# Kernel tuning notes

Hardware: AMD Instinct MI355X
Metric: run time of the kernel (lower is better)

The kernel has to match this reference:

```python
import jax, jax.numpy as jnp
import numpy as np
import math

# Config constants (match init_kwargs)
E = 8          # n_experts
TOPK = 2       # attn_topk
DIM = 1024     # transformer_dim
B = 4          # batch_size
S = 1024       # max_seq_len
H = 1024       # num_heads * head_dim
SCALE = 1.0 / math.sqrt(DIM)  # original divides scores by sqrt(self.dim)


def setup_inputs() -> dict:
    key = jax.random.key(0)
    ks = jax.random.split(key, 8)
    w = 0.02  # weight init scale
    return {
        "X": jax.random.normal(ks[0], (B, S, DIM), jnp.float32),
        "mask": jnp.ones((B, S), jnp.float32),
        "switch_W": jax.random.normal(ks[1], (DIM * S, E), jnp.float32) * w,
        "switch_b": jnp.zeros((E,), jnp.float32),
        "Wq": jax.random.normal(ks[2], (E, DIM, H), jnp.float32) * w,
        "bq": jnp.zeros((E, H), jnp.float32),
        "Wk": jax.random.normal(ks[3], (E, DIM, H), jnp.float32) * w,
        "bk": jnp.zeros((E, H), jnp.float32),
        "Wv": jax.random.normal(ks[4], (E, DIM, H), jnp.float32) * w,
        "bv": jnp.zeros((E, H), jnp.float32),
        "Wff": jax.random.normal(ks[5], (E, H, DIM), jnp.float32) * w,
        "bff": jnp.zeros((E, DIM), jnp.float32),
    }


def _dispatch_mask(route_prob):
    # top-k expert routing per batch element -> hard {0,1} mask [B, E]
    _, idx = jax.lax.top_k(route_prob, TOPK)  # [B, TOPK]
    b = route_prob.shape[0]
    return jnp.zeros((b, E), route_prob.dtype).at[jnp.arange(b)[:, None], idx].set(1.0)


def reference(X, mask, switch_W, switch_b, Wq, bq, Wk, bk, Wv, bv, Wff, bff):
    b, s, d = X.shape
    # Router: Linear(dim*seq_len -> n_experts) + softmax; preprocess -> idx_list
    logits = X.reshape(b, -1) @ switch_W + switch_b          # [B, E]
    route_prob = jax.nn.softmax(logits, axis=-1)
    m = _dispatch_mask(route_prob)                            # [B, E] dispatch mask (idx_list)

    # Per-expert Q/K/V projections (ColumnParallelLinearWithMoE over routed batches)
    Q = jnp.einsum('bsd,edh->ebsh', X, Wq) + bq[:, None, None, :]  # [E,B,S,H]
    K = jnp.einsum('bsd,edh->ebsh', X, Wk) + bk[:, None, None, :]
    V = jnp.einsum('bsd,edh->ebsh', X, Wv) + bv[:, None, None, :]

    # RowParallelMatmulWithMoE: per-expert scores, softmax (dropout p=0)
    scores = jnp.einsum('ebsh,ebth->ebst', Q, K) * SCALE      # [E,B,S,S]
    P = jax.nn.softmax(scores, axis=-1)

    # index_add_ combine of per-expert attn maps (second preprocess reuses same routing)
    A = jnp.einsum('be,ebst->bst', m, P)                      # [B,S,S]

    # ColumnParallelMatmulWithMoE: attn @ V per expert
    ctx = jnp.einsum('bst,ebth->ebsh', A, V)                  # [E,B,S,H]

    # RowParallelLinearWithMoE output projection, then index_add_ combine
    out = jnp.einsum('ebsh,ehd->ebsd', ctx, Wff) + bff[:, None, None, :]
    y = jnp.einsum('be,ebsd->bsd', m, out)                    # [B,S,DIM]
    return y
```

## Files before the change

### kernel.cpp

```cpp
#include <hip/hip_runtime.h>
#include <math.h>

typedef unsigned short u16;
typedef __attribute__((ext_vector_type(8))) short bffrag;
typedef __attribute__((ext_vector_type(4))) float f32x4;
typedef __attribute__((ext_vector_type(4))) unsigned short us4;
typedef __attribute__((ext_vector_type(8))) unsigned short us8;

#define SCALE_QK (1.0f/32.0f)

__device__ __forceinline__ u16 f2bf(float f) {
    unsigned u = __builtin_bit_cast(unsigned, f);
    u += 0x7fffu + ((u >> 16) & 1u);
    return (u16)(u >> 16);
}
__device__ __forceinline__ float bf2f(u16 v) {
    unsigned u = ((unsigned)v) << 16;
    return __builtin_bit_cast(float, u);
}

__device__ __forceinline__ void gld16(const u16* g, u16* l) {
    __builtin_amdgcn_global_load_lds(
        (const __attribute__((address_space(1))) void*)g,
        (__attribute__((address_space(3))) void*)l, 16, 0, 0);
}

__global__ __launch_bounds__(256) void router_partial(const float* __restrict__ X,
                                                      const float* __restrict__ sW,
                                                      float* __restrict__ part) {
    float acc[32];
    #pragma unroll
    for (int a = 0; a < 32; ++a) acc[a] = 0.f;
    int tid = blockIdx.x * 256 + threadIdx.x;
    #pragma unroll
    for (int q = 0; q < 4; ++q) {
        int i = tid + q * 262144;
        float4 w0 = *(const float4*)(sW + (size_t)i * 8);
        float4 w1 = *(const float4*)(sW + (size_t)i * 8 + 4);
        #pragma unroll
        for (int b = 0; b < 4; ++b) {
            float x = X[((size_t)b << 20) + i];
            acc[b*8+0] += x * w0.x; acc[b*8+1] += x * w0.y;
            acc[b*8+2] += x * w0.z; acc[b*8+3] += x * w0.w;
            acc[b*8+4] += x * w1.x; acc[b*8+5] += x * w1.y;
            acc[b*8+6] += x * w1.z; acc[b*8+7] += x * w1.w;
        }
    }
    __shared__ float wsum[4][32];
    int lane = threadIdx.x & 63, wv = threadIdx.x >> 6;
    #pragma unroll
    for (int a = 0; a < 32; ++a) {
        float v = acc[a];
        #pragma unroll
        for (int off = 32; off; off >>= 1) v += __shfl_down(v, off, 64);
        if (lane == 0) wsum[wv][a] = v;
    }
    __syncthreads();
    int t = threadIdx.x;
    if (t < 32)
        part[(size_t)t * 1024 + blockIdx.x] = wsum[0][t] + wsum[1][t] + wsum[2][t] + wsum[3][t];
}

__global__ __launch_bounds__(256) void router_final(const float* __restrict__ part,
                                                    const float* __restrict__ sb,
                                                    int* __restrict__ sel_need) {
    __shared__ float ps[32][8];
    __shared__ float lg[32];
    int t = threadIdx.x, a = t >> 3, c = t & 7;
    {
        float s = 0.f;
        const float* p = part + (size_t)a * 1024 + c * 128;
        for (int i = 0; i < 128; ++i) s += p[i];
        ps[a][c] = s;
    }
    __syncthreads();
    if (t < 32) {
        float v = 0.f;
        #pragma unroll
        for (int j = 0; j < 8; ++j) v += ps[t][j];
        lg[t] = v + sb[t & 7];
    }
    __syncthreads();
    if (t < 4) {
        int base = t * 8;
        int e1 = 0; float v1 = lg[base];
        for (int e = 1; e < 8; ++e) { if (lg[base + e] > v1) { v1 = lg[base + e]; e1 = e; } }
        int e2 = -1; float v2 = -INFINITY;
        for (int e = 0; e < 8; ++e) {
            if (e == e1) continue;
            if (lg[base + e] > v2) { v2 = lg[base + e]; e2 = e; }
        }
        sel_need[t * 2] = e1; sel_need[t * 2 + 1] = e2;
    }
    __syncthreads();
    if (t < 8) {
        int need = 0;
        for (int j = 0; j < 8; ++j) need |= (sel_need[j] == t);
        sel_need[8 + t] = need;
    }
}

__global__ __launch_bounds__(256) void c1_partial(const float* __restrict__ Wff,
        const float* __restrict__ bv, const int* __restrict__ sel_need,
        float* __restrict__ cpart) {
    int e = blockIdx.z;
    if (!sel_need[8 + e]) return;
    int d = blockIdx.x * 256 + threadIdx.x;
    int h0 = blockIdx.y * 128;
    const float* W = Wff + ((size_t)e << 20) + (size_t)h0 * 1024 + d;
    const float* bvp = bv + e * 1024 + h0;
    float s = 0.f;
    #pragma unroll 4
    for (int h = 0; h < 128; ++h) s += bvp[h] * W[(size_t)h * 1024];
    cpart[(e * 8 + blockIdx.y) * 1024 + d] = s;
}

__global__ __launch_bounds__(256) void ybias_kernel(const float* __restrict__ cpart,
        const float* __restrict__ bff, const int* __restrict__ sel,
        float* __restrict__ ybias) {
    int b = blockIdx.y;
    int d = blockIdx.x * 256 + threadIdx.x;
    int e0 = sel[b * 2], e1 = sel[b * 2 + 1];
    float c0 = 0.f, c1v = 0.f;
    #pragma unroll
    for (int hc = 0; hc < 8; ++hc) {
        c0  += cpart[(e0 * 8 + hc) * 1024 + d];
        c1v += cpart[(e1 * 8 + hc) * 1024 + d];
    }
    ybias[b * 1024 + d] = 2.f * (c0 + c1v) + bff[e0 * 1024 + d] + bff[e1 * 1024 + d];
}

__global__ __launch_bounds__(256) void cvt_misc(const float* __restrict__ X,
                                                const float* __restrict__ Wv,
                                                const int* __restrict__ sel_need,
                                                u16* __restrict__ Xb, u16* __restrict__ WvB) {
    int yz = blockIdx.y;
    const float* src; u16* dst;
    if (yz < 4) {
        src = X + ((size_t)yz << 20);  dst = Xb + ((size_t)yz << 20);
    } else {
        int e = yz - 4;
        if (!sel_need[8 + e]) return;
        src = Wv + ((size_t)e << 20);  dst = WvB + ((size_t)e << 20);
    }
    size_t i = (size_t)(blockIdx.x * 256 + threadIdx.x) * 8;
    float4 a = *(const float4*)(src + i);
    float4 b = *(const float4*)(src + i + 4);
    us8 o;
    o[0] = f2bf(a.x); o[1] = f2bf(a.y); o[2] = f2bf(a.z); o[3] = f2bf(a.w);
    o[4] = f2bf(b.x); o[5] = f2bf(b.y); o[6] = f2bf(b.z); o[7] = f2bf(b.w);
    *(us8*)(dst + i) = o;
}

__global__ __launch_bounds__(256) void cvt_wt(const float* __restrict__ Wq,
                                              const float* __restrict__ Wk,
                                              const float* __restrict__ Wff,
                                              const int* __restrict__ sel_need,
                                              u16* __restrict__ WqT, u16* __restrict__ WkT,
                                              u16* __restrict__ WffT) {
    int z = blockIdx.z;
    int type = z >> 3, e = z & 7;
    if (!sel_need[8 + e]) return;
    const float* src = (type == 0 ? Wq : type == 1 ? Wk : Wff) + ((size_t)e << 20);
    u16* dst = (type == 0 ? WqT : type == 1 ? WkT : WffT) + ((size_t)e << 20);
    __shared__ u16 lt[128 * 136];
    int R0 = blockIdx.y * 128, C0 = blockIdx.x * 128;
    int t = threadIdx.x;
    int c = t & 127;
    int rh = (t >> 7) * 4;
    #pragma unroll
    for (int it = 0; it < 16; ++it) {
        int r4 = it * 8 + rh;
        us4 o;
        #pragma unroll
        for (int j = 0; j < 4; ++j)
            o[j] = f2bf(src[(size_t)(R0 + r4 + j) * 1024 + C0 + c]);
        *(us4*)&lt[c * 136 + r4] = o;
    }
    __syncthreads();
    int dd = (t & 15) * 8;
    int hh = t >> 4;
    #pragma unroll
    for (int it = 0; it < 8; ++it) {
        int cr = it * 16 + hh;
        us8 o = *(const us8*)&lt[cr * 136 + dd];
        *(us8*)(dst + (size_t)(C0 + cr) * 1024 + R0 + dd) = o;
    }
}

__device__ __forceinline__ void stage_half8(const u16* g, int ld, u16* ldst, int tid) {
    int r = tid >> 3;
    int j = ((tid ^ r) & 7) * 8;
    gld16(g + (size_t)r * ld + j, ldst + tid * 8);
    gld16(g + (size_t)(r + 64) * ld + j, ldst + 4096 + tid * 8);
}

template<int Q, bool LASTVM>
__device__ __forceinline__ void phase8(const u16* Ac, const bffrag (&bfr)[4][2],
                                       f32x4 (&acc)[8][4], int rb, int l15, int x0,
                                       const u16* sg, int sld, u16* sdst, int tid) {
    bffrag af[2][2];
    #pragma unroll
    for (int mm = 0; mm < 2; ++mm) {
        int r = (rb + Q * 32 + mm * 16 + l15) * 64;
        af[mm][0] = *(const bffrag*)(Ac + r + x0);
        af[mm][1] = *(const bffrag*)(Ac + r + (x0 ^ 32));
    }
    __builtin_amdgcn_sched_barrier(0);
    stage_half8(sg, sld, sdst, tid);
    __builtin_amdgcn_sched_barrier(0);
    __builtin_amdgcn_s_barrier();
    asm volatile("s_waitcnt lgkmcnt(0)" ::: "memory");
    __builtin_amdgcn_sched_barrier(0);
    __builtin_amdgcn_s_setprio(1);
    #pragma unroll
    for (int ks = 0; ks < 2; ++ks)
        #pragma unroll
        for (int mm = 0; mm < 2; ++mm)
            #pragma unroll
            for (int nn = 0; nn < 4; ++nn)
                acc[Q*2+mm][nn] = __builtin_amdgcn_mfma_f32_16x16x32_bf16(
                    af[mm][ks], bfr[nn][ks], acc[Q*2+mm][nn], 0, 0, 0);
    __builtin_amdgcn_s_setprio(0);
    __builtin_amdgcn_sched_barrier(0);
    if (LASTVM) asm volatile("s_waitcnt vmcnt(4)" ::: "memory");
    __builtin_amdgcn_s_barrier();
}

__device__ __forceinline__ void gemm8(const u16* __restrict__ A, int lda,
                                      const u16* __restrict__ B, int ldb,
                                      int K, f32x4 (&acc)[8][4]) {
    __shared__ u16 lds[65536];
    const int tid = threadIdx.x, l = tid & 63, wid = tid >> 6;
    const int wr = wid >> 2, wc = wid & 3;
    const int l15 = l & 15;
    const int rb = wr * 128;
    const int cb = wc * 64;
    const int x0 = (((l >> 4) ^ (l & 7)) * 8);
    const int m0 = blockIdx.y * 256, n0 = blockIdx.x * 256;
    const int nt = K >> 6;

    const u16* Ag = A + (size_t)m0 * lda;
    const u16* Bg = B + (size_t)n0 * ldb;

    stage_half8(Ag,                          lda, lds,                 tid);
    stage_half8(Ag + (size_t)128 * lda,      lda, lds + 8192,          tid);
    stage_half8(Bg,                          ldb, lds + 16384,         tid);
    stage_half8(Bg + (size_t)128 * ldb,      ldb, lds + 16384 + 8192,  tid);
    stage_half8(Bg + 64,                     ldb, lds + 32768 + 16384, tid);
    stage_half8(Bg + 64 + (size_t)128 * ldb, ldb, lds + 32768 + 16384 + 8192, tid);
    asm volatile("s_waitcnt vmcnt(4)" ::: "memory");
    __builtin_amdgcn_s_barrier();

    for (int t7 = 0; t7 < nt; ++t7) {
        const int cur = t7 & 1;
        u16* Ac = lds + cur * 32768;
        u16* Bc = Ac + 16384;
        u16* An = lds + (cur ^ 1) * 32768;
        const int ka = (t7 + 1 < nt ? t7 + 1 : nt - 1) << 6;
        const int kb = (t7 + 2 < nt ? t7 + 2 : nt - 1) << 6;
        const u16* sA0 = Ag + ka;
        const u16* sA1 = Ag + (size_t)128 * lda + ka;
        const u16* sB0 = Bg + kb;
        const u16* sB1 = Bg + (size_t)128 * ldb + kb;

        bffrag bfr[4][2];
        #pragma unroll
        for (int nn = 0; nn < 4; ++nn) {
            int r = (cb + nn * 16 + l15) * 64;
            bfr[nn][0] = *(const bffrag*)(Bc + r + x0);
            bfr[nn][1] = *(const bffrag*)(Bc + r + (x0 ^ 32));
        }
        phase8<0, false>(Ac, bfr, acc, rb, l15, x0, sA0, lda, An, tid);
        phase8<1, false>(Ac, bfr, acc, rb, l15, x0, sA1, lda, An + 8192, tid);
        phase8<2, false>(Ac, bfr, acc, rb, l15, x0, sB0, ldb, Bc, tid);
        phase8<3, true >(Ac, bfr, acc, rb, l15, x0, sB1, ldb, Bc + 8192, tid);
    }
}

__device__ __forceinline__ void zero8(f32x4 (&acc)[8][4]) {
    #pragma unroll
    for (int m = 0; m < 8; ++m)
        #pragma unroll
        for (int n = 0; n < 4; ++n)
            #pragma unroll
            for (int i = 0; i < 4; ++i) acc[m][n][i] = 0.f;
}

__device__ __forceinline__ void epi8_bf16(u16* __restrict__ C, int ldc, float scale,
                                          const f32x4 (&acc)[8][4],
                                          const float* __restrict__ biasN) {
    const int tid = threadIdx.x, l = tid & 63, wid = tid >> 6;
    const int wr = wid >> 2, wc = wid & 3;
    const int m0 = blockIdx.y * 256 + wr * 128, n0 = blockIdx.x * 256 + wc * 64;
    const int l15 = l & 15, l4 = (l >> 4) * 4;
    #pragma unroll
    for (int mt = 0; mt < 8; ++mt)
        #pragma unroll
        for (int nn = 0; nn < 4; ++nn) {
            int col = n0 + nn * 16 + l15;
            float bn = biasN ? biasN[col] : 0.f;
            #pragma unroll
            for (int i = 0; i < 4; ++i) {
                int row = m0 + mt * 16 + l4 + i;
                C[(size_t)row * ldc + col] = f2bf(acc[mt][nn][i] * scale + bn);
            }
        }
}

__global__ __launch_bounds__(512) void mfma8_qk(const u16* __restrict__ Xb,
        const u16* __restrict__ WqT, const u16* __restrict__ WkT,
        const float* __restrict__ bq, const float* __restrict__ bk,
        const int* __restrict__ sel, u16* __restrict__ Qb, u16* __restrict__ Kb) {
    int z = blockIdx.z, w = z >> 3, bs = z & 7;
    int b = bs >> 1, e = sel[bs];
    f32x4 acc[8][4]; zero8(acc);
    gemm8(Xb + ((size_t)b << 20), 1024, (w ? WkT : WqT) + ((size_t)e << 20), 1024, 1024, acc);
    epi8_bf16((w ? Kb : Qb) + ((size_t)bs << 20), 1024, 1.0f, acc, (w ? bk : bq) + e * 1024);
}

__global__ __launch_bounds__(512) void mfma8_sw(const u16* __restrict__ Qb,
        const u16* __restrict__ Kb, const u16* __restrict__ WffT,
        const u16* __restrict__ WvB, const int* __restrict__ sel,
        u16* __restrict__ Sb, u16* __restrict__ P0b, u16* __restrict__ P1b) {
    int z = blockIdx.z;
    f32x4 acc[8][4]; zero8(acc);
    if (z < 8) {
        gemm8(Qb + ((size_t)z << 20), 1024, Kb + ((size_t)z << 20), 1024, 1024, acc);
        epi8_bf16(Sb + ((size_t)z << 20), 1024, SCALE_QK, acc, nullptr);
    } else {
        int h = (z >= 12), b = z & 3, e = sel[b * 2 + h];
        gemm8(WffT + ((size_t)e << 20), 1024, WvB + ((size_t)e << 20), 1024, 1024, acc);
        epi8_bf16((h ? P1b : P0b) + ((size_t)b << 20), 1024, 1.0f, acc, nullptr);
    }
}

__global__ __launch_bounds__(256) void wvfadd(const u16* __restrict__ P0b,
                                              const u16* __restrict__ P1b,
                                              u16* __restrict__ W) {
    size_t i = (size_t)(blockIdx.x * 256 + threadIdx.x) * 8;
    us8 a = *(const us8*)(P0b + i);
    us8 b = *(const us8*)(P1b + i);
    us8 o;
    #pragma unroll
    for (int j = 0; j < 8; ++j) o[j] = f2bf(bf2f(a[j]) + bf2f(b[j]));
    *(us8*)(W + i) = o;
}

__device__ __forceinline__ void stage_tile(const u16* a0, const u16* a1,
                                           const u16* b0, const u16* b1,
                                           u16* sa, u16* sb, int tid) {
    gld16(a0, &sa[tid * 8]);
    gld16(a1, &sa[2048 + tid * 8]);
    gld16(b0, &sb[tid * 8]);
    gld16(b1, &sb[2048 + tid * 8]);
}

__device__ __forceinline__ void gemm_ds(const u16* __restrict__ A, int lda,
                                        const u16* __restrict__ B, int ldb,
                                        int K, f32x4 (&acc)[4][4]) {
    __shared__ u16 sA[2][4096];
    __shared__ u16 sB[2][4096];
    const int tid = threadIdx.x, lane = tid & 63, wv = tid >> 6;
    const int wr = (wv >> 1) * 64, wc = (wv & 1) * 64;
    const int l15 = lane & 15, lk = (lane >> 4) * 8;
    const int m0 = blockIdx.y * 128, n0 = blockIdx.x * 128;
    const int r0 = tid >> 2, k8 = (tid & 3) * 8;

    const u16* a0 = A + (size_t)(m0 + r0) * lda + k8;
    const u16* a1 = A + (size_t)(m0 + 64 + r0) * lda + k8;
    const u16* b0 = B + (size_t)(n0 + r0) * ldb + k8;
    const u16* b1 = B + (size_t)(n0 + 64 + r0) * ldb + k8;

    stage_tile(a0, a1, b0, b1, sA[0], sB[0], tid);
    __syncthreads();

    const int nt = K >> 5;
    for (int t = 0; t < nt; ++t) {
        const int cur = t & 1;
        if (t + 1 < nt) {
            int k0 = (t + 1) << 5;
            stage_tile(a0 + k0, a1 + k0, b0 + k0, b1 + k0, sA[cur ^ 1], sB[cur ^ 1], tid);
        }
        bffrag av[4], bf[4];
        #pragma unroll
        for (int m = 0; m < 4; ++m)
            av[m] = *reinterpret_cast<const bffrag*>(&sA[cur][(wr + m * 16 + l15) * 32 + lk]);
        #pragma unroll
        for (int n = 0; n < 4; ++n)
            bf[n] = *reinterpret_cast<const bffrag*>(&sB[cur][(wc + n * 16 + l15) * 32 + lk]);
        #pragma unroll
        for (int m = 0; m < 4; ++m)
            #pragma unroll
            for (int n = 0; n < 4; ++n)
                acc[m][n] = __builtin_amdgcn_mfma_f32_16x16x32_bf16(av[m], bf[n], acc[m][n], 0, 0, 0);
        __syncthreads();
    }
}

__device__ __forceinline__ void zero_acc(f32x4 (&acc)[4][4]) {
    #pragma unroll
    for (int m = 0; m < 4; ++m)
        #pragma unroll
        for (int n = 0; n < 4; ++n)
            #pragma unroll
            for (int i = 0; i < 4; ++i) acc[m][n][i] = 0.f;
}

__device__ __forceinline__ void epilogue_bf16(u16* __restrict__ C, int ldc,
                                              const f32x4 (&acc)[4][4]) {
    const int tid = threadIdx.x, lane = tid & 63, wv = tid >> 6;
    const int wr = (wv >> 1) * 64, wc = (wv & 1) * 64;
    const int m0 = blockIdx.y * 128, n0 = blockIdx.x * 128;
    const int l15 = lane & 15, l4 = (lane >> 4) * 4;
    #pragma unroll
    for (int m = 0; m < 4; ++m)
        #pragma unroll
        for (int n = 0; n < 4; ++n) {
            int col = n0 + wc + n * 16 + l15;
            #pragma unroll
            for (int i = 0; i < 4; ++i) {
                int row = m0 + wr + m * 16 + l4 + i;
                C[(size_t)row * ldc + col] = f2bf(acc[m][n][i]);
            }
        }
}

__device__ __forceinline__ void epilogue_f32(float* __restrict__ C, int ldc,
                                             const f32x4 (&acc)[4][4],
                                             const float* __restrict__ bias1) {
    const int tid = threadIdx.x, lane = tid & 63, wv = tid >> 6;
    const int wr = (wv >> 1) * 64, wc = (wv & 1) * 64;
    const int m0 = blockIdx.y * 128, n0 = blockIdx.x * 128;
    const int l15 = lane & 15, l4 = (lane >> 4) * 4;
    #pragma unroll
    for (int m = 0; m < 4; ++m)
        #pragma unroll
        for (int n = 0; n < 4; ++n) {
            int col = n0 + wc + n * 16 + l15;
            float bn = bias1 ? bias1[col] : 0.f;
            #pragma unroll
            for (int i = 0; i < 4; ++i) {
                int row = m0 + wr + m * 16 + l4 + i;
                C[(size_t)row * ldc + col] = acc[m][n][i] + bn;
            }
        }
}

__global__ __launch_bounds__(256) void sm_combine(const u16* __restrict__ Sb, u16* __restrict__ Ab) {
    int bs = blockIdx.x, b = bs >> 10, s = bs & 1023;
    const u16* S0 = Sb + ((size_t)(b * 2) << 20) + (size_t)s * 1024;
    const u16* S1 = S0 + (1u << 20);
    int t = threadIdx.x, lane = t & 63, wv = t >> 6;
    us4 xv0 = *(const us4*)(S0 + t * 4);
    us4 xv1 = *(const us4*)(S1 + t * 4);
    float x0[4], x1[4];
    #pragma unroll
    for (int j = 0; j < 4; ++j) { x0[j] = bf2f(xv0[j]); x1[j] = bf2f(xv1[j]); }
    float m0 = fmaxf(fmaxf(x0[0], x0[1]), fmaxf(x0[2], x0[3]));
    float m1 = fmaxf(fmaxf(x1[0], x1[1]), fmaxf(x1[2], x1[3]));
    #pragma unroll
    for (int off = 32; off; off >>= 1) {
        m0 = fmaxf(m0, __shfl_xor(m0, off, 64));
        m1 = fmaxf(m1, __shfl_xor(m1, off, 64));
    }
    __shared__ float wred[4][4];
    if (lane == 0) { wred[wv][0] = m0; wred[wv][1] = m1; }
    __syncthreads();
    m0 = fmaxf(fmaxf(wred[0][0], wred[1][0]), fmaxf(wred[2][0], wred[3][0]));
    m1 = fmaxf(fmaxf(wred[0][1], wred[1][1]), fmaxf(wred[2][1], wred[3][1]));
    float e0[4], e1[4];
    #pragma unroll
    for (int j = 0; j < 4; ++j) { e0[j] = __expf(x0[j] - m0); e1[j] = __expf(x1[j] - m1); }
    float s0 = e0[0] + e0[1] + e0[2] + e0[3];
    float s1 = e1[0] + e1[1] + e1[2] + e1[3];
    #pragma unroll
    for (int off = 32; off; off >>= 1) {
        s0 += __shfl_xor(s0, off, 64);
        s1 += __shfl_xor(s1, off, 64);
    }
    if (lane == 0) { wred[wv][2] = s0; wred[wv][3] = s1; }
    __syncthreads();
    s0 = wred[0][2] + wred[1][2] + wred[2][2] + wred[3][2];
    s1 = wred[0][3] + wred[1][3] + wred[2][3] + wred[3][3];
    float r0 = 1.f / s0, r1 = 1.f / s1;
    us4 o;
    #pragma unroll
    for (int j = 0; j < 4; ++j) o[j] = f2bf(e0[j] * r0 + e1[j] * r1);
    *(us4*)(Ab + ((size_t)b << 20) + (size_t)s * 1024 + t * 4) = o;
}

__global__ __launch_bounds__(256) void mfma_mt(const u16* __restrict__ Wvfsum,
        const u16* __restrict__ Xb, u16* __restrict__ Mtb) {
    int b = blockIdx.z;
    f32x4 acc[4][4]; zero_acc(acc);
    gemm_ds(Wvfsum + ((size_t)b << 20), 1024, Xb + ((size_t)b << 20), 1024, 1024, acc);
    epilogue_bf16(Mtb + ((size_t)b << 20), 1024, acc);
}

__global__ __launch_bounds__(256) void mfma_y(const u16* __restrict__ Abf,
        const u16* __restrict__ Mtb, const float* __restrict__ ybias,
        float* __restrict__ y) {
    int b = blockIdx.z;
    f32x4 acc[4][4]; zero_acc(acc);
    gemm_ds(Abf + ((size_t)b << 20), 1024, Mtb + ((size_t)b << 20), 1024, 1024, acc);
    epilogue_f32(y + ((size_t)b << 20), 1024, acc, ybias + b * 1024);
}

extern "C" void kernel_launch(void* const* d_in, const int* in_sizes, int n_in,
                              void* d_out, int out_size, void* d_ws, size_t ws_size,
                              hipStream_t stream) {
    const float* X   = (const float*)d_in[0];
    const float* sW  = (const float*)d_in[2];
    const float* sb  = (const float*)d_in[3];
    const float* Wq  = (const float*)d_in[4];
    const float* bq  = (const float*)d_in[5];
    const float* Wk  = (const float*)d_in[6];
    const float* bk  = (const float*)d_in[7];
    const float* Wv  = (const float*)d_in[8];
    const float* bv  = (const float*)d_in[9];
    const float* Wff = (const float*)d_in[10];
    const float* bff = (const float*)d_in[11];
    float* y = (float*)d_out;

    char* w = (char*)d_ws;
    float* part  = (float*)w;
    float* cpart = (float*)w;
    int*   sel   = (int*)(w + (1u << 18));
    float* ybias = (float*)(w + (1u << 18) + 256);
    u16* base = (u16*)(w + (1u << 19));
    u16* Xb   = base;
    u16* WqT  = Xb   + (4u << 20);
    u16* WkT  = WqT  + (8u << 20);
    u16* WffT = WkT  + (8u << 20);
    u16* WvB  = WffT + (8u << 20);
    u16* Qb   = WvB  + (8u << 20);
    u16* Kb   = Qb   + (8u << 20);
    u16* Sb   = Kb   + (8u << 20);
    u16* P0b  = Sb   + (8u << 20);
    u16* P1b  = P0b  + (4u << 20);
    u16* Abf    = WqT;
    u16* Mtb    = WkT;
    u16* Wvfsum = Qb;

    router_partial<<<1024, 256, 0, stream>>>(X, sW, part);
    router_final<<<1, 256, 0, stream>>>(part, sb, sel);
    c1_partial<<<dim3(4, 8, 8), 256, 0, stream>>>(Wff, bv, sel, cpart);
    ybias_kernel<<<dim3(4, 4), 256, 0, stream>>>(cpart, bff, sel, ybias);
    cvt_misc<<<dim3(512, 12), 256, 0, stream>>>(X, Wv, sel, Xb, WvB);
    cvt_wt<<<dim3(8, 8, 24), 256, 0, stream>>>(Wq, Wk, Wff, sel, WqT, WkT, WffT);

    mfma8_qk<<<dim3(4, 4, 16), 512, 0, stream>>>(Xb, WqT, WkT, bq, bk, sel, Qb, Kb);
    mfma8_sw<<<dim3(4, 4, 16), 512, 0, stream>>>(Qb, Kb, WffT, WvB, sel, Sb, P0b, P1b);
    wvfadd<<<2048, 256, 0, stream>>>(P0b, P1b, Wvfsum);
    mfma_mt<<<dim3(8, 8, 4), 256, 0, stream>>>(Wvfsum, Xb, Mtb);
    sm_combine<<<4096, 256, 0, stream>>>(Sb, Abf);
    mfma_y<<<dim3(8, 8, 4), 256, 0, stream>>>(Abf, Mtb, ybias, y);
}
```

Measured before the change: 221.8 us.

## Fuse two-expert WvWff GEMMs by K-concatenation and halve the gemm8 pipeline phases

The two per-batch expert products WffT·WvB are now computed as one GEMM with K=2048. The K loop switches from the first expert's operands to the second's at a split point, so the summed result is written directly. This removes the separate wvfadd kernel and the P0/P1 intermediate buffers, and shrinks the mfma8_sw grid from 16 to 12 z-slices. The gemm8 main loop also goes from four quarter-tile phases to two full-tile phases, each staging a whole 256-row tile, which means fewer barriers per K step. In exchange, the fused blocks do twice the K work, which lengthens the critical path of that launch, and each phase holds more A fragments in registers.

```diff
diff --git a/kernel.cpp b/kernel.cpp
--- a/kernel.cpp
+++ b/kernel.cpp
@@ -188,26 +188,29 @@
     }
 }
 
-__device__ __forceinline__ void stage_half8(const u16* g, int ld, u16* ldst, int tid) {
+__device__ __forceinline__ void stage_full(const u16* g, int ld, u16* ldst, int tid) {
     int r = tid >> 3;
     int j = ((tid ^ r) & 7) * 8;
-    gld16(g + (size_t)r * ld + j, ldst + tid * 8);
-    gld16(g + (size_t)(r + 64) * ld + j, ldst + 4096 + tid * 8);
-}
-
-template<int Q, bool LASTVM>
-__device__ __forceinline__ void phase8(const u16* Ac, const bffrag (&bfr)[4][2],
+    const u16* gr = g + (size_t)r * ld + j;
+    gld16(gr,                      ldst + tid * 8);
+    gld16(gr + (size_t)64  * ld,   ldst + 4096  + tid * 8);
+    gld16(gr + (size_t)128 * ld,   ldst + 8192  + tid * 8);
+    gld16(gr + (size_t)192 * ld,   ldst + 12288 + tid * 8);
+}
+
+template<int QB, bool LASTVM>
+__device__ __forceinline__ void phaseF(const u16* Ac, const bffrag (&bfr)[4][2],
                                        f32x4 (&acc)[8][4], int rb, int l15, int x0,
                                        const u16* sg, int sld, u16* sdst, int tid) {
-    bffrag af[2][2];
-    #pragma unroll
-    for (int mm = 0; mm < 2; ++mm) {
-        int r = (rb + Q * 32 + mm * 16 + l15) * 64;
+    bffrag af[4][2];
+    #pragma unroll
+    for (int mm = 0; mm < 4; ++mm) {
+        int r = (rb + QB * 64 + mm * 16 + l15) * 64;
         af[mm][0] = *(const bffrag*)(Ac + r + x0);
         af[mm][1] = *(const bffrag*)(Ac + r + (x0 ^ 32));
     }
     __builtin_amdgcn_sched_barrier(0);
-    stage_half8(sg, sld, sdst, tid);
+    stage_full(sg, sld, sdst, tid);
     __builtin_amdgcn_sched_barrier(0);
     __builtin_amdgcn_s_barrier();
     asm volatile("s_waitcnt lgkmcnt(0)" ::: "memory");
@@ -216,19 +219,21 @@
     #pragma unroll
     for (int ks = 0; ks < 2; ++ks)
         #pragma unroll
-        for (int mm = 0; mm < 2; ++mm)
+        for (int mm = 0; mm < 4; ++mm)
             #pragma unroll
             for (int nn = 0; nn < 4; ++nn)
-                acc[Q*2+mm][nn] = __builtin_amdgcn_mfma_f32_16x16x32_bf16(
-                    af[mm][ks], bfr[nn][ks], acc[Q*2+mm][nn], 0, 0, 0);
+                acc[QB*4+mm][nn] = __builtin_amdgcn_mfma_f32_16x16x32_bf16(
+                    af[mm][ks], bfr[nn][ks], acc[QB*4+mm][nn], 0, 0, 0);
     __builtin_amdgcn_s_setprio(0);
     __builtin_amdgcn_sched_barrier(0);
     if (LASTVM) asm volatile("s_waitcnt vmcnt(4)" ::: "memory");
     __builtin_amdgcn_s_barrier();
 }
 
-__device__ __forceinline__ void gemm8(const u16* __restrict__ A, int lda,
-                                      const u16* __restrict__ B, int ldb,
+__device__ __forceinline__ void gemm8(const u16* __restrict__ A0, const u16* __restrict__ A1,
+                                      int asplit, int lda,
+                                      const u16* __restrict__ B0, const u16* __restrict__ B1,
+                                      int bsplit, int ldb,
                                       int K, f32x4 (&acc)[8][4]) {
     __shared__ u16 lds[65536];
     const int tid = threadIdx.x, l = tid & 63, wid = tid >> 6;
@@ -240,15 +245,18 @@
     const int m0 = blockIdx.y * 256, n0 = blockIdx.x * 256;
     const int nt = K >> 6;
 
-    const u16* Ag = A + (size_t)m0 * lda;
-    const u16* Bg = B + (size_t)n0 * ldb;
-
-    stage_half8(Ag,                          lda, lds,                 tid);
-    stage_half8(Ag + (size_t)128 * lda,      lda, lds + 8192,          tid);
-    stage_half8(Bg,                          ldb, lds + 16384,         tid);
-    stage_half8(Bg + (size_t)128 * ldb,      ldb, lds + 16384 + 8192,  tid);
-    stage_half8(Bg + 64,                     ldb, lds + 32768 + 16384, tid);
-    stage_half8(Bg + 64 + (size_t)128 * ldb, ldb, lds + 32768 + 16384 + 8192, tid);
+    const u16* A0g = A0 + (size_t)m0 * lda;
+    const u16* A1g = A1 + (size_t)m0 * lda;
+    const u16* B0g = B0 + (size_t)n0 * ldb;
+    const u16* B1g = B1 + (size_t)n0 * ldb;
+
+    stage_full(A0g, lda, lds,         tid);
+    stage_full(B0g, ldb, lds + 16384, tid);
+    {
+        int kb = (1 < nt ? 1 : nt - 1) << 6;
+        const u16* Bp = (kb < bsplit) ? B0g + kb : B1g + (kb - bsplit);
+        stage_full(Bp, ldb, lds + 32768 + 16384, tid);
+    }
     asm volatile("s_waitcnt vmcnt(4)" ::: "memory");
     __builtin_amdgcn_s_barrier();
 
@@ -257,12 +265,10 @@
         u16* Ac = lds + cur * 32768;
         u16* Bc = Ac + 16384;
         u16* An = lds + (cur ^ 1) * 32768;
-        const int ka = (t7 + 1 < nt ? t7 + 1 : nt - 1) << 6;
-        const int kb = (t7 + 2 < nt ? t7 + 2 : nt - 1) << 6;
-        const u16* sA0 = Ag + ka;
-        const u16* sA1 = Ag + (size_t)128 * lda + ka;
-        const u16* sB0 = Bg + kb;
-        const u16* sB1 = Bg + (size_t)128 * ldb + kb;
+        int ka = (t7 + 1 < nt ? t7 + 1 : nt - 1) << 6;
+        int kb = (t7 + 2 < nt ? t7 + 2 : nt - 1) << 6;
+        const u16* Ap = (ka < asplit) ? A0g + ka : A1g + (ka - asplit);
+        const u16* Bp = (kb < bsplit) ? B0g + kb : B1g + (kb - bsplit);
 
         bffrag bfr[4][2];
         #pragma unroll
@@ -271,10 +277,8 @@
             bfr[nn][0] = *(const bffrag*)(Bc + r + x0);
             bfr[nn][1] = *(const bffrag*)(Bc + r + (x0 ^ 32));
         }
-        phase8<0, false>(Ac, bfr, acc, rb, l15, x0, sA0, lda, An, tid);
-        phase8<1, false>(Ac, bfr, acc, rb, l15, x0, sA1, lda, An + 8192, tid);
-        phase8<2, false>(Ac, bfr, acc, rb, l15, x0, sB0, ldb, Bc, tid);
-        phase8<3, true >(Ac, bfr, acc, rb, l15, x0, sB1, ldb, Bc + 8192, tid);
+        phaseF<0, false>(Ac, bfr, acc, rb, l15, x0, Ap, lda, An, tid);
+        phaseF<1, true >(Ac, bfr, acc, rb, l15, x0, Bp, ldb, Bc, tid);
     }
 }
 
@@ -314,37 +318,31 @@
         const int* __restrict__ sel, u16* __restrict__ Qb, u16* __restrict__ Kb) {
     int z = blockIdx.z, w = z >> 3, bs = z & 7;
     int b = bs >> 1, e = sel[bs];
+    const u16* A = Xb + ((size_t)b << 20);
+    const u16* B = (w ? WkT : WqT) + ((size_t)e << 20);
     f32x4 acc[8][4]; zero8(acc);
-    gemm8(Xb + ((size_t)b << 20), 1024, (w ? WkT : WqT) + ((size_t)e << 20), 1024, 1024, acc);
+    gemm8(A, A, 1 << 30, 1024, B, B, 1 << 30, 1024, 1024, acc);
     epi8_bf16((w ? Kb : Qb) + ((size_t)bs << 20), 1024, 1.0f, acc, (w ? bk : bq) + e * 1024);
 }
 
 __global__ __launch_bounds__(512) void mfma8_sw(const u16* __restrict__ Qb,
         const u16* __restrict__ Kb, const u16* __restrict__ WffT,
         const u16* __restrict__ WvB, const int* __restrict__ sel,
-        u16* __restrict__ Sb, u16* __restrict__ P0b, u16* __restrict__ P1b) {
+        u16* __restrict__ Sb, u16* __restrict__ Wvfsum) {
     int z = blockIdx.z;
     f32x4 acc[8][4]; zero8(acc);
     if (z < 8) {
-        gemm8(Qb + ((size_t)z << 20), 1024, Kb + ((size_t)z << 20), 1024, 1024, acc);
+        const u16* A = Qb + ((size_t)z << 20);
+        const u16* B = Kb + ((size_t)z << 20);
+        gemm8(A, A, 1 << 30, 1024, B, B, 1 << 30, 1024, 1024, acc);
         epi8_bf16(Sb + ((size_t)z << 20), 1024, SCALE_QK, acc, nullptr);
     } else {
-        int h = (z >= 12), b = z & 3, e = sel[b * 2 + h];
-        gemm8(WffT + ((size_t)e << 20), 1024, WvB + ((size_t)e << 20), 1024, 1024, acc);
-        epi8_bf16((h ? P1b : P0b) + ((size_t)b << 20), 1024, 1.0f, acc, nullptr);
-    }
-}
-
-__global__ __launch_bounds__(256) void wvfadd(const u16* __restrict__ P0b,
-                                              const u16* __restrict__ P1b,
-                                              u16* __restrict__ W) {
-    size_t i = (size_t)(blockIdx.x * 256 + threadIdx.x) * 8;
-    us8 a = *(const us8*)(P0b + i);
-    us8 b = *(const us8*)(P1b + i);
-    us8 o;
-    #pragma unroll
-    for (int j = 0; j < 8; ++j) o[j] = f2bf(bf2f(a[j]) + bf2f(b[j]));
-    *(us8*)(W + i) = o;
+        int b = z - 8;
+        int e0 = sel[b * 2], e1 = sel[b * 2 + 1];
+        gemm8(WffT + ((size_t)e0 << 20), WffT + ((size_t)e1 << 20), 1024, 1024,
+              WvB  + ((size_t)e0 << 20), WvB  + ((size_t)e1 << 20), 1024, 1024, 2048, acc);
+        epi8_bf16(Wvfsum + ((size_t)b << 20), 1024, 1.0f, acc, nullptr);
+    }
 }
 
 __device__ __forceinline__ void stage_tile(const u16* a0, const u16* a1,
@@ -537,11 +535,9 @@
     u16* Qb   = WvB  + (8u << 20);
     u16* Kb   = Qb   + (8u << 20);
     u16* Sb   = Kb   + (8u << 20);
-    u16* P0b  = Sb   + (8u << 20);
-    u16* P1b  = P0b  + (4u << 20);
+    u16* Wvfsum = Sb + (8u << 20);
     u16* Abf    = WqT;
     u16* Mtb    = WkT;
-    u16* Wvfsum = Qb;
 
     router_partial<<<1024, 256, 0, stream>>>(X, sW, part);
     router_final<<<1, 256, 0, stream>>>(part, sb, sel);
@@ -551,8 +547,7 @@
     cvt_wt<<<dim3(8, 8, 24), 256, 0, stream>>>(Wq, Wk, Wff, sel, WqT, WkT, WffT);
 
     mfma8_qk<<<dim3(4, 4, 16), 512, 0, stream>>>(Xb, WqT, WkT, bq, bk, sel, Qb, Kb);
-    mfma8_sw<<<dim3(4, 4, 16), 512, 0, stream>>>(Qb, Kb, WffT, WvB, sel, Sb, P0b, P1b);
-    wvfadd<<<2048, 256, 0, stream>>>(P0b, P1b, Wvfsum);
+    mfma8_sw<<<dim3(4, 4, 12), 512, 0, stream>>>(Qb, Kb, WffT, WvB, sel, Sb, Wvfsum);
     mfma_mt<<<dim3(8, 8, 4), 256, 0, stream>>>(Wvfsum, Xb, Mtb);
     sm_combine<<<4096, 256, 0, stream>>>(Sb, Abf);
     mfma_y<<<dim3(8, 8, 4), 256, 0, stream>>>(Abf, Mtb, ybias, y);
```

New measurement: 233.0 us. +5.0%, slower.

## Merge conversion kernels and co-schedule Mt GEMM with softmax combine

Applied to the files above, without the earlier changes.

Merges the two fp32-to-bf16 conversion kernels into one launch using a shared 3D grid, so X/Wv blocks are tiled 128x128 alongside the transposing weight blocks. It also folds the Mt GEMM and the softmax-combine kernel into a single launch, where the first 256 blocks run the GEMM and the rest run the row softmax. The aim is to cut launch overhead and let the memory-bound softmax blocks fill the GPU while the small 256-block GEMM runs. The merged kernel now reserves the GEMM's shared-memory footprint for every block, which may lower occupancy for the softmax blocks.

```diff
diff --git a/kernel.cpp b/kernel.cpp
--- a/kernel.cpp
+++ b/kernel.cpp
@@ -130,61 +130,67 @@
     ybias[b * 1024 + d] = 2.f * (c0 + c1v) + bff[e0 * 1024 + d] + bff[e1 * 1024 + d];
 }
 
-__global__ __launch_bounds__(256) void cvt_misc(const float* __restrict__ X,
-                                                const float* __restrict__ Wv,
-                                                const int* __restrict__ sel_need,
-                                                u16* __restrict__ Xb, u16* __restrict__ WvB) {
-    int yz = blockIdx.y;
-    const float* src; u16* dst;
-    if (yz < 4) {
-        src = X + ((size_t)yz << 20);  dst = Xb + ((size_t)yz << 20);
-    } else {
-        int e = yz - 4;
-        if (!sel_need[8 + e]) return;
-        src = Wv + ((size_t)e << 20);  dst = WvB + ((size_t)e << 20);
-    }
-    size_t i = (size_t)(blockIdx.x * 256 + threadIdx.x) * 8;
-    float4 a = *(const float4*)(src + i);
-    float4 b = *(const float4*)(src + i + 4);
-    us8 o;
-    o[0] = f2bf(a.x); o[1] = f2bf(a.y); o[2] = f2bf(a.z); o[3] = f2bf(a.w);
-    o[4] = f2bf(b.x); o[5] = f2bf(b.y); o[6] = f2bf(b.z); o[7] = f2bf(b.w);
-    *(us8*)(dst + i) = o;
-}
-
-__global__ __launch_bounds__(256) void cvt_wt(const float* __restrict__ Wq,
-                                              const float* __restrict__ Wk,
-                                              const float* __restrict__ Wff,
-                                              const int* __restrict__ sel_need,
-                                              u16* __restrict__ WqT, u16* __restrict__ WkT,
-                                              u16* __restrict__ WffT) {
+__global__ __launch_bounds__(256) void cvt_all(const float* __restrict__ Wq,
+                                               const float* __restrict__ Wk,
+                                               const float* __restrict__ Wff,
+                                               const float* __restrict__ X,
+                                               const float* __restrict__ Wv,
+                                               const int* __restrict__ sel_need,
+                                               u16* __restrict__ WqT, u16* __restrict__ WkT,
+                                               u16* __restrict__ WffT,
+                                               u16* __restrict__ Xb, u16* __restrict__ WvB) {
     int z = blockIdx.z;
-    int type = z >> 3, e = z & 7;
-    if (!sel_need[8 + e]) return;
-    const float* src = (type == 0 ? Wq : type == 1 ? Wk : Wff) + ((size_t)e << 20);
-    u16* dst = (type == 0 ? WqT : type == 1 ? WkT : WffT) + ((size_t)e << 20);
-    __shared__ u16 lt[128 * 136];
     int R0 = blockIdx.y * 128, C0 = blockIdx.x * 128;
     int t = threadIdx.x;
-    int c = t & 127;
-    int rh = (t >> 7) * 4;
-    #pragma unroll
-    for (int it = 0; it < 16; ++it) {
-        int r4 = it * 8 + rh;
-        us4 o;
-        #pragma unroll
-        for (int j = 0; j < 4; ++j)
-            o[j] = f2bf(src[(size_t)(R0 + r4 + j) * 1024 + C0 + c]);
-        *(us4*)&lt[c * 136 + r4] = o;
-    }
-    __syncthreads();
-    int dd = (t & 15) * 8;
-    int hh = t >> 4;
-    #pragma unroll
-    for (int it = 0; it < 8; ++it) {
-        int cr = it * 16 + hh;
-        us8 o = *(const us8*)&lt[cr * 136 + dd];
-        *(us8*)(dst + (size_t)(C0 + cr) * 1024 + R0 + dd) = o;
+    if (z < 24) {
+        int type = z >> 3, e = z & 7;
+        if (!sel_need[8 + e]) return;
+        const float* src = (type == 0 ? Wq : type == 1 ? Wk : Wff) + ((size_t)e << 20);
+        u16* dst = (type == 0 ? WqT : type == 1 ? WkT : WffT) + ((size_t)e << 20);
+        __shared__ u16 lt[128 * 136];
+        int c = t & 127;
+        int rh = (t >> 7) * 4;
+        #pragma unroll
+        for (int it = 0; it < 16; ++it) {
+            int r4 = it * 8 + rh;
+            us4 o;
+            #pragma unroll
+            for (int j = 0; j < 4; ++j)
+                o[j] = f2bf(src[(size_t)(R0 + r4 + j) * 1024 + C0 + c]);
+            *(us4*)&lt[c * 136 + r4] = o;
+        }
+        __syncthreads();
+        int dd = (t & 15) * 8;
+        int hh = t >> 4;
+        #pragma unroll
+        for (int it = 0; it < 8; ++it) {
+            int cr = it * 16 + hh;
+            us8 o = *(const us8*)&lt[cr * 136 + dd];
+            *(us8*)(dst + (size_t)(C0 + cr) * 1024 + R0 + dd) = o;
+        }
+    } else {
+        const float* src; u16* dst;
+        if (z < 28) {
+            int b = z - 24;
+            src = X + ((size_t)b << 20);  dst = Xb + ((size_t)b << 20);
+        } else {
+            int e = z - 28;
+            if (!sel_need[8 + e]) return;
+            src = Wv + ((size_t)e << 20);  dst = WvB + ((size_t)e << 20);
+        }
+        int r = t >> 4;
+        int c8 = (t & 15) * 8;
+        #pragma unroll
+        for (int it = 0; it < 8; ++it) {
+            int row = R0 + it * 16 + r;
+            const float* sp = src + (size_t)row * 1024 + C0 + c8;
+            float4 a = *(const float4*)sp;
+            float4 b2 = *(const float4*)(sp + 4);
+            us8 o;
+            o[0] = f2bf(a.x); o[1] = f2bf(a.y); o[2] = f2bf(a.z); o[3] = f2bf(a.w);
+            o[4] = f2bf(b2.x); o[5] = f2bf(b2.y); o[6] = f2bf(b2.z); o[7] = f2bf(b2.w);
+            *(us8*)(dst + (size_t)row * 1024 + C0 + c8) = o;
+        }
     }
 }
 
@@ -358,13 +364,12 @@
 
 __device__ __forceinline__ void gemm_ds(const u16* __restrict__ A, int lda,
                                         const u16* __restrict__ B, int ldb,
-                                        int K, f32x4 (&acc)[4][4]) {
+                                        int K, int m0, int n0, f32x4 (&acc)[4][4]) {
     __shared__ u16 sA[2][4096];
     __shared__ u16 sB[2][4096];
     const int tid = threadIdx.x, lane = tid & 63, wv = tid >> 6;
     const int wr = (wv >> 1) * 64, wc = (wv & 1) * 64;
     const int l15 = lane & 15, lk = (lane >> 4) * 8;
-    const int m0 = blockIdx.y * 128, n0 = blockIdx.x * 128;
     const int r0 = tid >> 2, k8 = (tid & 3) * 8;
 
     const u16* a0 = A + (size_t)(m0 + r0) * lda + k8;
@@ -407,11 +412,10 @@
             for (int i = 0; i < 4; ++i) acc[m][n][i] = 0.f;
 }
 
-__device__ __forceinline__ void epilogue_bf16(u16* __restrict__ C, int ldc,
-                                              const f32x4 (&acc)[4][4]) {
+__device__ __forceinline__ void epi4_bf16(u16* __restrict__ C, int ldc, int m0, int n0,
+                                          const f32x4 (&acc)[4][4]) {
     const int tid = threadIdx.x, lane = tid & 63, wv = tid >> 6;
     const int wr = (wv >> 1) * 64, wc = (wv & 1) * 64;
-    const int m0 = blockIdx.y * 128, n0 = blockIdx.x * 128;
     const int l15 = lane & 15, l4 = (lane >> 4) * 4;
     #pragma unroll
     for (int m = 0; m < 4; ++m)
@@ -426,12 +430,11 @@
         }
 }
 
-__device__ __forceinline__ void epilogue_f32(float* __restrict__ C, int ldc,
-                                             const f32x4 (&acc)[4][4],
-                                             const float* __restrict__ bias1) {
+__device__ __forceinline__ void epi4_f32(float* __restrict__ C, int ldc, int m0, int n0,
+                                         const f32x4 (&acc)[4][4],
+                                         const float* __restrict__ bias1) {
     const int tid = threadIdx.x, lane = tid & 63, wv = tid >> 6;
     const int wr = (wv >> 1) * 64, wc = (wv & 1) * 64;
-    const int m0 = blockIdx.y * 128, n0 = blockIdx.x * 128;
     const int l15 = lane & 15, l4 = (lane >> 4) * 4;
     #pragma unroll
     for (int m = 0; m < 4; ++m)
@@ -447,8 +450,17 @@
         }
 }
 
-__global__ __launch_bounds__(256) void sm_combine(const u16* __restrict__ Sb, u16* __restrict__ Ab) {
-    int bs = blockIdx.x, b = bs >> 10, s = bs & 1023;
+__global__ __launch_bounds__(256) void sm_mt(const u16* __restrict__ Sb, u16* __restrict__ Ab,
+        const u16* __restrict__ Wvfsum, const u16* __restrict__ Xb, u16* __restrict__ Mtb) {
+    int bid = blockIdx.x;
+    if (bid < 256) {
+        int b = bid >> 6, m0 = ((bid >> 3) & 7) * 128, n0 = (bid & 7) * 128;
+        f32x4 acc[4][4]; zero_acc(acc);
+        gemm_ds(Wvfsum + ((size_t)b << 20), 1024, Xb + ((size_t)b << 20), 1024, 1024, m0, n0, acc);
+        epi4_bf16(Mtb + ((size_t)b << 20), 1024, m0, n0, acc);
+        return;
+    }
+    int bs = bid - 256, b = bs >> 10, s = bs & 1023;
     const u16* S0 = Sb + ((size_t)(b * 2) << 20) + (size_t)s * 1024;
     const u16* S1 = S0 + (1u << 20);
     int t = threadIdx.x, lane = t & 63, wv = t >> 6;
@@ -490,21 +502,14 @@
     *(us4*)(Ab + ((size_t)b << 20) + (size_t)s * 1024 + t * 4) = o;
 }
 
-__global__ __launch_bounds__(256) void mfma_mt(const u16* __restrict__ Wvfsum,
-        const u16* __restrict__ Xb, u16* __restrict__ Mtb) {
-    int b = blockIdx.z;
-    f32x4 acc[4][4]; zero_acc(acc);
-    gemm_ds(Wvfsum + ((size_t)b << 20), 1024, Xb + ((size_t)b << 20), 1024, 1024, acc);
-    epilogue_bf16(Mtb + ((size_t)b << 20), 1024, acc);
-}
-
 __global__ __launch_bounds__(256) void mfma_y(const u16* __restrict__ Abf,
         const u16* __restrict__ Mtb, const float* __restrict__ ybias,
         float* __restrict__ y) {
     int b = blockIdx.z;
+    int m0 = blockIdx.y * 128, n0 = blockIdx.x * 128;
     f32x4 acc[4][4]; zero_acc(acc);
-    gemm_ds(Abf + ((size_t)b << 20), 1024, Mtb + ((size_t)b << 20), 1024, 1024, acc);
-    epilogue_f32(y + ((size_t)b << 20), 1024, acc, ybias + b * 1024);
+    gemm_ds(Abf + ((size_t)b << 20), 1024, Mtb + ((size_t)b << 20), 1024, 1024, m0, n0, acc);
+    epi4_f32(y + ((size_t)b << 20), 1024, m0, n0, acc, ybias + b * 1024);
 }
 
 extern "C" void kernel_launch(void* const* d_in, const int* in_sizes, int n_in,
@@ -547,13 +552,11 @@
     router_final<<<1, 256, 0, stream>>>(part, sb, sel);
     c1_partial<<<dim3(4, 8, 8), 256, 0, stream>>>(Wff, bv, sel, cpart);
     ybias_kernel<<<dim3(4, 4), 256, 0, stream>>>(cpart, bff, sel, ybias);
-    cvt_misc<<<dim3(512, 12), 256, 0, stream>>>(X, Wv, sel, Xb, WvB);
-    cvt_wt<<<dim3(8, 8, 24), 256, 0, stream>>>(Wq, Wk, Wff, sel, WqT, WkT, WffT);
+    cvt_all<<<dim3(8, 8, 36), 256, 0, stream>>>(Wq, Wk, Wff, X, Wv, sel, WqT, WkT, WffT, Xb, WvB);
 
     mfma8_qk<<<dim3(4, 4, 16), 512, 0, stream>>>(Xb, WqT, WkT, bq, bk, sel, Qb, Kb);
     mfma8_sw<<<dim3(4, 4, 16), 512, 0, stream>>>(Qb, Kb, WffT, WvB, sel, Sb, P0b, P1b);
     wvfadd<<<2048, 256, 0, stream>>>(P0b, P1b, Wvfsum);
-    mfma_mt<<<dim3(8, 8, 4), 256, 0, stream>>>(Wvfsum, Xb, Mtb);
-    sm_combine<<<4096, 256, 0, stream>>>(Sb, Abf);
+    sm_mt<<<4352, 256, 0, stream>>>(Sb, Abf, Wvfsum, Xb, Mtb);
     mfma_y<<<dim3(8, 8, 4), 256, 0, stream>>>(Abf, Mtb, ybias, y);
 }
```

Result: no change. 219.5 us (-1.0%).
